# Kernel optimization log

Hardware: AMD Instinct MI355X
Metric: run time of the kernel (lower is better)

Reference implementation:

```python
import jax, jax.numpy as jnp
import numpy as np

EMB = 1024

def setup_inputs() -> dict:
    key = jax.random.key(0)
    ks = jax.random.split(key, 7)
    s = 1.0 / np.sqrt(EMB)
    x = jax.random.normal(ks[0], (4, 2048, EMB), dtype=jnp.float32)
    Wk = jax.random.normal(ks[1], (EMB, EMB), dtype=jnp.float32) * s
    bk = jnp.zeros((EMB,), dtype=jnp.float32)
    Wq = jax.random.normal(ks[2], (EMB, EMB), dtype=jnp.float32) * s
    bq = jnp.zeros((EMB,), dtype=jnp.float32)
    Wv = jax.random.normal(ks[3], (EMB, EMB), dtype=jnp.float32) * s
    bv = jnp.zeros((EMB,), dtype=jnp.float32)
    return {"x": x, "Wk": Wk, "bk": bk, "Wq": Wq, "bq": bq, "Wv": Wv, "bv": bv}

def reference(x, Wk, bk, Wq, bq, Wv, bv):
    # Linear layers: x @ W.T + b (torch nn.Linear convention)
    k = jnp.einsum('bse,fe->bsf', x, Wk) + bk
    q = jnp.einsum('bse,fe->bsf', x, Wq) + bq
    v = jnp.einsum('bse,fe->bsf', x, Wv) + bv
    E = x.shape[-1]
    # NOTE: original computes k @ q^T (not q @ k^T) — reproduce faithfully.
    sim = jnp.einsum('bsd,btd->bst', k, q) / jnp.sqrt(jnp.float32(E))
    S = x.shape[1]
    causal = jnp.tril(jnp.ones((S, S), dtype=bool))  # [S,S]
    sim = jnp.where(causal, sim, -jnp.inf)
    attn = jax.nn.softmax(sim, axis=-1)
    return jnp.einsum('bst,btd->bsd', attn, v)
```

## Files before the change

kernel.cpp:

```cpp
#include <hip/hip_runtime.h>
#include <cstdint>


typedef __attribute__((ext_vector_type(8))) _Float16 f16x8;
typedef __attribute__((ext_vector_type(4))) float f32x4;

__device__ __forceinline__ unsigned short f2h(float x) {
  return __builtin_bit_cast(unsigned short, (_Float16)x);
}

__device__ __forceinline__ void lds_dma16(const void* g, void* l) {
  auto gp = reinterpret_cast<const __attribute__((address_space(1))) void*>(
      reinterpret_cast<uintptr_t>(g));
  auto lp = reinterpret_cast<__attribute__((address_space(3))) void*>(
      reinterpret_cast<uintptr_t>(l));
  __builtin_amdgcn_global_load_lds(gp, lp, 16, 0, 0);
}

__device__ __forceinline__ void gemm128(const unsigned short* __restrict__ Ag,
                                        const unsigned short* __restrict__ Bg,
                                        int lda, int ldb, int nk,
                                        unsigned short* As, unsigned short* Bs,
                                        f32x4 acc[4][4]) {
  const int tid = threadIdx.x;
  const int lane = tid & 63, wave = tid >> 6;
  const int wm = wave >> 1, wn = wave & 1;
  const int sr = lane >> 2;
  const int scb = (((lane & 3) ^ ((lane >> 3) & 3)) * 8);
  const int rr = lane & 15, qq = lane >> 4;
  const int slot = ((qq ^ ((rr >> 1) & 3)) * 8);

#pragma unroll
  for (int i = 0; i < 4; ++i)
#pragma unroll
    for (int j = 0; j < 4; ++j) {
      f32x4 z = {0.f, 0.f, 0.f, 0.f};
      acc[i][j] = z;
    }

#pragma unroll
  for (int c = 0; c < 2; ++c) {
    int chunk = wave * 2 + c;
    int row = chunk * 16 + sr;
    lds_dma16(Ag + (size_t)row * lda + scb, As + chunk * 512);
    lds_dma16(Bg + (size_t)row * ldb + scb, Bs + chunk * 512);
  }

  int buf = 0;
  for (int k0 = 0; k0 < nk; k0 += 32) {
    __syncthreads();
    const int kn = k0 + 32;
    if (kn < nk) {
      unsigned short* An = As + (buf ^ 1) * 4096;
      unsigned short* Bn = Bs + (buf ^ 1) * 4096;
#pragma unroll
      for (int c = 0; c < 2; ++c) {
        int chunk = wave * 2 + c;
        int row = chunk * 16 + sr;
        lds_dma16(Ag + (size_t)row * lda + kn + scb, An + chunk * 512);
        lds_dma16(Bg + (size_t)row * ldb + kn + scb, Bn + chunk * 512);
      }
    }

    f16x8 af[4], bf[4];
    const unsigned short* Ar = As + buf * 4096 + (wm * 64 + rr) * 32 + slot;
    const unsigned short* Br = Bs + buf * 4096 + (wn * 64 + rr) * 32 + slot;
#pragma unroll
    for (int i = 0; i < 4; ++i) af[i] = *(const f16x8*)(Ar + i * 512);
#pragma unroll
    for (int j = 0; j < 4; ++j) bf[j] = *(const f16x8*)(Br + j * 512);
#pragma unroll
    for (int i = 0; i < 4; ++i)
#pragma unroll
      for (int j = 0; j < 4; ++j)
        acc[i][j] = __builtin_amdgcn_mfma_f32_16x16x32_f16(af[i], bf[j],
                                                           acc[i][j], 0, 0, 0);
    buf ^= 1;
  }
}

__device__ __forceinline__ void gemm128_k64(
    const unsigned short* __restrict__ Ag, const unsigned short* __restrict__ Bg,
    int lda, int ldb, int nk, unsigned short* As, unsigned short* Bs,
    f32x4 acc[4][4]) {
  const int tid = threadIdx.x;
  const int lane = tid & 63, wave = tid >> 6;
  const int wm = wave >> 1, wn = wave & 1;
  const int sr = lane >> 3;
  const int scb = ((lane & 7) ^ sr) * 8;
  const int rr = lane & 15, qq = lane >> 4;
  const int slot0 = ((qq) ^ (rr & 7)) * 8;
  const int slot1 = ((4 + qq) ^ (rr & 7)) * 8;

#pragma unroll
  for (int i = 0; i < 4; ++i)
#pragma unroll
    for (int j = 0; j < 4; ++j) {
      f32x4 z = {0.f, 0.f, 0.f, 0.f};
      acc[i][j] = z;
    }

#pragma unroll
  for (int c = 0; c < 4; ++c) {
    int chunk = wave * 4 + c;
    int row = chunk * 8 + sr;
    lds_dma16(Ag + (size_t)row * lda + scb, As + chunk * 512);
    lds_dma16(Bg + (size_t)row * ldb + scb, Bs + chunk * 512);
  }

  int buf = 0;
  for (int k0 = 0; k0 < nk; k0 += 64) {
    __syncthreads();
    const int kn = k0 + 64;
    if (kn < nk) {
      unsigned short* An = As + (buf ^ 1) * 8192;
      unsigned short* Bn = Bs + (buf ^ 1) * 8192;
#pragma unroll
      for (int c = 0; c < 4; ++c) {
        int chunk = wave * 4 + c;
        int row = chunk * 8 + sr;
        lds_dma16(Ag + (size_t)row * lda + kn + scb, An + chunk * 512);
        lds_dma16(Bg + (size_t)row * ldb + kn + scb, Bn + chunk * 512);
      }
    }

    const unsigned short* Ar = As + buf * 8192 + (wm * 64 + rr) * 64;
    const unsigned short* Br = Bs + buf * 8192 + (wn * 64 + rr) * 64;
    {
      f16x8 af[4], bf[4];
#pragma unroll
      for (int i = 0; i < 4; ++i) af[i] = *(const f16x8*)(Ar + i * 1024 + slot0);
#pragma unroll
      for (int j = 0; j < 4; ++j) bf[j] = *(const f16x8*)(Br + j * 1024 + slot0);
#pragma unroll
      for (int i = 0; i < 4; ++i)
#pragma unroll
        for (int j = 0; j < 4; ++j)
          acc[i][j] = __builtin_amdgcn_mfma_f32_16x16x32_f16(af[i], bf[j],
                                                             acc[i][j], 0, 0, 0);
    }
    {
      f16x8 af[4], bf[4];
#pragma unroll
      for (int i = 0; i < 4; ++i) af[i] = *(const f16x8*)(Ar + i * 1024 + slot1);
#pragma unroll
      for (int j = 0; j < 4; ++j) bf[j] = *(const f16x8*)(Br + j * 1024 + slot1);
#pragma unroll
      for (int i = 0; i < 4; ++i)
#pragma unroll
        for (int j = 0; j < 4; ++j)
          acc[i][j] = __builtin_amdgcn_mfma_f32_16x16x32_f16(af[i], bf[j],
                                                             acc[i][j], 0, 0, 0);
    }
    buf ^= 1;
  }
}

__global__ void cvt_kernel(const float* __restrict__ x,
                           const float* __restrict__ w0,
                           const float* __restrict__ w1,
                           const float* __restrict__ w2,
                           unsigned short* __restrict__ dst,
                           float* __restrict__ rsum) {
  int i = blockIdx.x * 256 + threadIdx.x;
  if (i >= 2883584) {
    int z2 = i - 2883584;
    float4 z = {0.f, 0.f, 0.f, 0.f};
    ((float4*)rsum)[z2] = z;
    return;
  }
  const float* s;
  size_t si;
  if (i < 2097152) {
    s = x; si = i;
  } else {
    int j = i - 2097152;
    int z = j >> 18;
    s = (z == 0) ? w0 : ((z == 1) ? w1 : w2);
    si = j & 262143;
  }
  float4 f = ((const float4*)s)[si];
  ushort4 u;
  u.x = f2h(f.x); u.y = f2h(f.y); u.z = f2h(f.z); u.w = f2h(f.w);
  ((ushort4*)dst)[i] = u;
}

__global__ __launch_bounds__(256) void qkv_gemm_kernel(
    const unsigned short* __restrict__ xh, const unsigned short* __restrict__ wh,
    const float* __restrict__ bk, const float* __restrict__ bq,
    const float* __restrict__ bv, unsigned short* __restrict__ kh,
    unsigned short* __restrict__ qh, unsigned short* __restrict__ vT) {
  __shared__ unsigned short As[2 * 128 * 32], Bs[2 * 128 * 32];
  const int tn = blockIdx.x & 7, z = blockIdx.x >> 3;
  const unsigned short* W = wh + (size_t)z * 1048576;
  const int tm = blockIdx.y;

  const unsigned short* Ag = (z == 2) ? (W + (size_t)tn * 128 * 1024)
                                      : (xh + (size_t)tm * 128 * 1024);
  const unsigned short* Bg = (z == 2) ? (xh + (size_t)tm * 128 * 1024)
                                      : (W + (size_t)tn * 128 * 1024);

  f32x4 acc[4][4];
  gemm128(Ag, Bg, 1024, 1024, 1024, As, Bs, acc);

  const int lane = threadIdx.x & 63, wave = threadIdx.x >> 6;
  const int wm = wave >> 1, wn = wave & 1, rr = lane & 15, qq = lane >> 4;

  if (z == 2) {
#pragma unroll
    for (int i = 0; i < 4; ++i) {
      int d0 = tn * 128 + wm * 64 + i * 16 + qq * 4;
      float4 bi = *(const float4*)(bv + d0);
      float bir[4] = {bi.x, bi.y, bi.z, bi.w};
#pragma unroll
      for (int reg = 0; reg < 4; ++reg) {
        int d = d0 + reg;
#pragma unroll
        for (int j = 0; j < 4; ++j) {
          int tg = tm * 128 + wn * 64 + j * 16 + rr;
          int bb = tg >> 11, tt = tg & 2047;
          vT[((size_t)(bb * 1024 + d)) * 2048 + tt] =
              f2h(acc[i][j][reg] + bir[reg]);
        }
      }
    }
  } else {
    const float* bias = (z == 0) ? bk : bq;
    unsigned short* dst = (z == 0) ? kh : qh;
    float bj[4];
#pragma unroll
    for (int j = 0; j < 4; ++j)
      bj[j] = bias[tn * 128 + wn * 64 + j * 16 + rr];
#pragma unroll
    for (int i = 0; i < 4; ++i)
#pragma unroll
      for (int reg = 0; reg < 4; ++reg) {
        int gm = tm * 128 + wm * 64 + i * 16 + qq * 4 + reg;
#pragma unroll
        for (int j = 0; j < 4; ++j) {
          int gc = tn * 128 + wn * 64 + j * 16 + rr;
          dst[(size_t)gm * 1024 + gc] = f2h(acc[i][j][reg] + bj[j]);
        }
      }
  }
}

__global__ __launch_bounds__(256) void scores_kernel(
    const unsigned short* __restrict__ kh, const unsigned short* __restrict__ qh,
    unsigned short* __restrict__ P, float* __restrict__ rsum) {
  const int b = blockIdx.y;
  int idx = blockIdx.x;
  int ts = (int)((sqrtf(8.0f * idx + 1.0f) - 1.0f) * 0.5f);
  while ((ts + 1) * (ts + 2) / 2 <= idx) ++ts;
  while (ts * (ts + 1) / 2 > idx) --ts;
  const int tt = idx - ts * (ts + 1) / 2;
  __shared__ unsigned short As[2 * 128 * 64], Bs[2 * 128 * 64];

  f32x4 acc[4][4];
  gemm128_k64(kh + ((size_t)(b * 2048 + ts * 128)) * 1024,
              qh + ((size_t)(b * 2048 + tt * 128)) * 1024,
              1024, 1024, 1024, As, Bs, acc);

  const int lane = threadIdx.x & 63, wave = threadIdx.x >> 6;
  const int wm = wave >> 1, wn = wave & 1, rr = lane & 15, qq = lane >> 4;
  unsigned short* Pb = P + (size_t)b * 2048 * 2048;
  float* rs = rsum + b * 2048;
#pragma unroll
  for (int i = 0; i < 4; ++i)
#pragma unroll
    for (int reg = 0; reg < 4; ++reg) {
      int srow = ts * 128 + wm * 64 + i * 16 + qq * 4 + reg;
      float p = 0.f;
#pragma unroll
      for (int j = 0; j < 4; ++j) {
        int tcol = tt * 128 + wn * 64 + j * 16 + rr;
        float e = (tcol <= srow) ? __expf(acc[i][j][reg] * 0.03125f - 4.0f)
                                 : 0.0f;
        Pb[(size_t)srow * 2048 + tcol] = f2h(e);
        p += e;
      }
#pragma unroll
      for (int off = 1; off < 16; off <<= 1) p += __shfl_xor(p, off);
      if (rr == 0) atomicAdd(rs + srow, p);
    }
}

__global__ __launch_bounds__(256) void pv_gemm_kernel(
    const unsigned short* __restrict__ P, const unsigned short* __restrict__ vT,
    const float* __restrict__ rsum, float* __restrict__ out) {
  const int td = blockIdx.x, ts = 15 - blockIdx.y, b = blockIdx.z;
  __shared__ unsigned short As[2 * 128 * 64], Bs[2 * 128 * 64];

  f32x4 acc[4][4];
  gemm128_k64(P + ((size_t)(b * 2048 + ts * 128)) * 2048,
              vT + ((size_t)(b * 1024 + td * 128)) * 2048,
              2048, 2048, (ts + 1) * 128, As, Bs, acc);

  const int lane = threadIdx.x & 63, wave = threadIdx.x >> 6;
  const int wm = wave >> 1, wn = wave & 1, rr = lane & 15, qq = lane >> 4;
#pragma unroll
  for (int i = 0; i < 4; ++i) {
    int s0 = ts * 128 + wm * 64 + i * 16 + qq * 4;
    float4 r4 = *(const float4*)(rsum + b * 2048 + s0);
    float rv[4] = {__builtin_amdgcn_rcpf(r4.x), __builtin_amdgcn_rcpf(r4.y),
                   __builtin_amdgcn_rcpf(r4.z), __builtin_amdgcn_rcpf(r4.w)};
#pragma unroll
    for (int reg = 0; reg < 4; ++reg) {
      int srow = s0 + reg;
#pragma unroll
      for (int j = 0; j < 4; ++j) {
        int dcol = td * 128 + wn * 64 + j * 16 + rr;
        out[((size_t)(b * 2048 + srow)) * 1024 + dcol] =
            acc[i][j][reg] * rv[reg];
      }
    }
  }
}

extern "C" void kernel_launch(void* const* d_in, const int* in_sizes, int n_in,
                              void* d_out, int out_size, void* d_ws,
                              size_t ws_size, hipStream_t stream) {
  const float* x  = (const float*)d_in[0];
  const float* Wk = (const float*)d_in[1];
  const float* bk = (const float*)d_in[2];
  const float* Wq = (const float*)d_in[3];
  const float* bq = (const float*)d_in[4];
  const float* Wv = (const float*)d_in[5];
  const float* bv = (const float*)d_in[6];
  float* out = (float*)d_out;

  char* ws = (char*)d_ws;
  const size_t MB = 1ull << 20;
  unsigned short* xh = (unsigned short*)(ws + 0);
  unsigned short* wh = (unsigned short*)(ws + 16 * MB);
  unsigned short* P  = (unsigned short*)(ws + 0);
  unsigned short* kh = (unsigned short*)(ws + 38 * MB);
  unsigned short* qh = (unsigned short*)(ws + 54 * MB);
  unsigned short* vT = (unsigned short*)(ws + 70 * MB);
  float* rsum = (float*)(ws + 86 * MB);

  cvt_kernel<<<11272, 256, 0, stream>>>(x, Wk, Wq, Wv, xh, rsum);
  qkv_gemm_kernel<<<dim3(24, 64), 256, 0, stream>>>(xh, wh, bk, bq, bv,
                                                    kh, qh, vT);
  scores_kernel<<<dim3(136, 4), 256, 0, stream>>>(kh, qh, P, rsum);
  pv_gemm_kernel<<<dim3(8, 16, 4), 256, 0, stream>>>(P, vT, rsum, out);
}
```

Before: 239.9 us.

## Split long causal PV row tiles across two blocks with atomic accumulation

Row tiles 8-15 of the P·V GEMM, the ones with the longest causal K ranges, are split into two partial K ranges handled by separate blocks. A lookup table orders the 24 work items longest first to balance load. Split tiles accumulate into the output with float atomics, so the cvt kernel now zeroes the lower half of each batch's output beforehand. This shortens the critical-path block for better wave balance, at the cost of extra atomic traffic, an extra zeroing pass, and non-deterministic float summation order.

```diff
diff --git a/kernel.cpp b/kernel.cpp
--- a/kernel.cpp
+++ b/kernel.cpp
@@ -161,12 +161,18 @@
                            const float* __restrict__ w1,
                            const float* __restrict__ w2,
                            unsigned short* __restrict__ dst,
-                           float* __restrict__ rsum) {
+                           float* __restrict__ rsum,
+                           float* __restrict__ out) {
   int i = blockIdx.x * 256 + threadIdx.x;
+  const float4 z4 = {0.f, 0.f, 0.f, 0.f};
+  if (i >= 2885632) {
+    int j = i - 2885632;
+    int b = j >> 18, r = j & 262143;
+    ((float4*)out)[(size_t)b * 524288 + 262144 + r] = z4;
+    return;
+  }
   if (i >= 2883584) {
-    int z2 = i - 2883584;
-    float4 z = {0.f, 0.f, 0.f, 0.f};
-    ((float4*)rsum)[z2] = z;
+    ((float4*)rsum)[i - 2883584] = z4;
     return;
   }
   const float* s;
@@ -288,16 +294,24 @@
 __global__ __launch_bounds__(256) void pv_gemm_kernel(
     const unsigned short* __restrict__ P, const unsigned short* __restrict__ vT,
     const float* __restrict__ rsum, float* __restrict__ out) {
-  const int td = blockIdx.x, ts = 15 - blockIdx.y, b = blockIdx.z;
+  static const signed char TSx[24] = {15,15,14,7, 14,13,13,12,6,
+                                      12,11,11,10,5, 10,9,9,8,4, 8,3,2,1,0};
+  static const signed char T0x[24] = {0,8,0,0, 8,0,7,0,0,
+                                      7,0,6,0,0, 6,0,5,0,0, 5,0,0,0,0};
+  static const signed char NTx[24] = {8,8,8,8, 7,7,7,7,7,
+                                      6,6,6,6,6, 5,5,5,5,5, 4,4,3,2,1};
+  const int td = blockIdx.x, y = blockIdx.y, b = blockIdx.z;
+  const int ts = TSx[y], t0 = T0x[y], nt = NTx[y];
   __shared__ unsigned short As[2 * 128 * 64], Bs[2 * 128 * 64];
 
   f32x4 acc[4][4];
-  gemm128_k64(P + ((size_t)(b * 2048 + ts * 128)) * 2048,
-              vT + ((size_t)(b * 1024 + td * 128)) * 2048,
-              2048, 2048, (ts + 1) * 128, As, Bs, acc);
+  gemm128_k64(P + ((size_t)(b * 2048 + ts * 128)) * 2048 + t0 * 128,
+              vT + ((size_t)(b * 1024 + td * 128)) * 2048 + t0 * 128,
+              2048, 2048, nt * 128, As, Bs, acc);
 
   const int lane = threadIdx.x & 63, wave = threadIdx.x >> 6;
   const int wm = wave >> 1, wn = wave & 1, rr = lane & 15, qq = lane >> 4;
+  const bool split = (ts >= 8);
 #pragma unroll
   for (int i = 0; i < 4; ++i) {
     int s0 = ts * 128 + wm * 64 + i * 16 + qq * 4;
@@ -310,8 +324,10 @@
 #pragma unroll
       for (int j = 0; j < 4; ++j) {
         int dcol = td * 128 + wn * 64 + j * 16 + rr;
-        out[((size_t)(b * 2048 + srow)) * 1024 + dcol] =
-            acc[i][j][reg] * rv[reg];
+        size_t ofs = ((size_t)(b * 2048 + srow)) * 1024 + dcol;
+        float v = acc[i][j][reg] * rv[reg];
+        if (split) atomicAdd(out + ofs, v);
+        else out[ofs] = v;
       }
     }
   }
@@ -339,9 +355,9 @@
   unsigned short* vT = (unsigned short*)(ws + 70 * MB);
   float* rsum = (float*)(ws + 86 * MB);
 
-  cvt_kernel<<<11272, 256, 0, stream>>>(x, Wk, Wq, Wv, xh, rsum);
+  cvt_kernel<<<15368, 256, 0, stream>>>(x, Wk, Wq, Wv, xh, rsum, out);
   qkv_gemm_kernel<<<dim3(24, 64), 256, 0, stream>>>(xh, wh, bk, bq, bv,
                                                     kh, qh, vT);
   scores_kernel<<<dim3(136, 4), 256, 0, stream>>>(kh, qh, P, rsum);
-  pv_gemm_kernel<<<dim3(8, 16, 4), 256, 0, stream>>>(P, vT, rsum, out);
-}
+  pv_gemm_kernel<<<dim3(8, 24, 4), 256, 0, stream>>>(P, vT, rsum, out);
+}
```

Result: slower. 255.1 us (+6.3%).
